# Kernel tuning notes

Measured on AMD Instinct MI355X. Metric: run time of the kernel, lower is better.

## Reference

```python
import math
import jax, jax.numpy as jnp
import numpy as np

D_MODEL, STATE_DIM, SEQ_L = 256, 64, 8192


def setup_inputs() -> dict:
    key = jax.random.key(0)
    ks = jax.random.split(key, 6)
    d, N = D_MODEL, STATE_DIM
    s = 1.0 / math.sqrt(N)
    return {
        "Lambda_re": jax.random.normal(ks[0], (d, N), jnp.float32),
        "Lambda_im": jax.random.normal(ks[1], (d, N), jnp.float32),
        "P_re": jax.random.normal(ks[2], (d, N), jnp.float32) * s,
        "P_im": jax.random.normal(ks[3], (d, N), jnp.float32) * s,
        "B_re": jax.random.normal(ks[4], (d, N), jnp.float32) * s,
        "B_im": jnp.zeros((d, N), jnp.float32),
        "log_dt": jax.random.uniform(ks[5], (d,), jnp.float32,
                                     math.log(1e-3), math.log(0.1)),
        "D": jnp.zeros((d,), jnpp := jnp.float32) if False else jnp.zeros((d,), jnp.float32),
        "L": SEQ_L,
    }


def reference(Lambda_re, Lambda_im, P_re, P_im, B_re, B_im, log_dt, D, L):
    # NPLR / Cauchy-Woodbury S4 kernel (learn_cd=False -> C = B, D is a zero buffer)
    Lam = (-jax.nn.softplus(Lambda_re) + 1j * Lambda_im).astype(jnp.complex64)  # [d, N]
    P = (P_re + 1j * P_im).astype(jnp.complex64)                                # [d, N]
    B = (B_re + 1j * B_im).astype(jnp.complex64)                                # [d, N]
    dt = jnp.exp(log_dt)                                                        # [d]

    k = jnp.arange(L)
    z = jnp.exp((-2j * jnp.pi / L) * k).astype(jnp.complex64)                   # [L] roots of unity
    eps = jnp.finfo(jnp.float32).eps
    denom_z = 1.0 + z
    denom_z = jnp.where(jnp.abs(denom_z) < eps, jnp.complex64(eps), denom_z)

    # Bilinear-transform frequencies g: [d, L] complex
    g = (2.0 / dt)[:, None] * ((1.0 - z) / denom_z)[None, :]

    # Cauchy resolvent R: [d, L, N] complex (the dominant intermediate)
    R = 1.0 / (g[:, :, None] - Lam[:, None, :])

    Pc, Bc = jnp.conj(P), jnp.conj(B)
    PRB = jnp.einsum('dn,dln,dn->dl', Pc, R, B)
    PRP = jnp.einsum('dn,dln,dn->dl', Pc, R, P)
    BRB = jnp.einsum('dn,dln,dn->dl', Bc, R, B)
    BRP = jnp.einsum('dn,dln,dn->dl', Bc, R, P)

    # Woodbury rank-1 correction, then undo the bilinear prefactor
    K_hat = (2.0 / denom_z)[None, :] * (BRB - BRP * PRB / (1.0 + PRP))          # [d, L]
    K = jnp.fft.ifft(K_hat, n=L, axis=-1).real.astype(jnp.float32)
    return (K, D)
```

## Files before the change

kernel.cpp:

```cpp
#include <hip/hip_runtime.h>
#include <math.h>

#ifndef M_PI
#define M_PI 3.14159265358979323846
#endif

#define DMODEL 256
#define NSTATE 64
#define LSEQ   8192
#define INVL   (1.0f/8192.0f)

#define OFF_TW  0
#define OFF_DN  (6144*8)
#define OFF_CDT (OFF_DN + DMODEL*NSTATE*32)

__device__ __forceinline__ float sin_rev(float r) {
#if __has_builtin(__builtin_amdgcn_sinf)
  return __builtin_amdgcn_sinf(r);
#else
  return __sinf(r * 6.283185307179586f);
#endif
}
__device__ __forceinline__ float cos_rev(float r) {
#if __has_builtin(__builtin_amdgcn_cosf)
  return __builtin_amdgcn_cosf(r);
#else
  return __cosf(r * 6.283185307179586f);
#endif
}

__device__ __forceinline__ float2 cmul(float2 a, float2 b) {
  return make_float2(a.x*b.x - a.y*b.y, a.x*b.y + a.y*b.x);
}

__device__ __forceinline__ float2 woodbury(float2 S1, float2 S2, float2 S3,
                                           float2 S4, float T) {
  float nr = (S1.x*S1.x - S1.y*S1.y) + (S2.x*S2.x - S2.y*S2.y);
  float ni = 2.0f*(S1.x*S1.y + S2.x*S2.y);
  float dr = 1.0f + S3.x, di = S3.y;
  float inv = __builtin_amdgcn_rcpf(fmaf(dr, dr, di*di));
  float qr = (nr*dr + ni*di) * inv;
  float qi = (ni*dr - nr*di) * inv;
  float vr = S4.x - qr, vi = S4.y - qi;
  return make_float2((vr - T*vi)*INVL, (vi + T*vr)*INVL);
}

__global__ __launch_bounds__(256) void precompute_kernel(
    const float* __restrict__ Lre, const float* __restrict__ Lim,
    const float* __restrict__ Pre, const float* __restrict__ Pim,
    const float* __restrict__ Bre, const float* __restrict__ Bim,
    const float* __restrict__ log_dt, char* __restrict__ ws)
{
  const int t = blockIdx.x * blockDim.x + threadIdx.x;
  float2* tw  = (float2*)(ws + OFF_TW);
  float4* dn  = (float4*)(ws + OFF_DN);
  float*  cdt = (float*)(ws + OFF_CDT);

  if (t < 6144) {
    double th = (2.0 * M_PI / (double)LSEQ) * (double)t;
    double s, c; sincos(th, &s, &c);
    tw[t] = make_float2((float)c, (float)s);
  }
  {
    float lre = Lre[t], lim = Lim[t];
    float pre = Pre[t], pim = Pim[t];
    float bre = Bre[t], bim = Bim[t];
    float sp = fmaxf(lre, 0.0f) + log1pf(expf(-fabsf(lre)));
    float w1r = pre*bre + pim*bim;
    float w1i = pre*bim - pim*bre;
    float w2  = pre*pre + pim*pim;
    float w3  = bre*bre + bim*bim;
    dn[2*t]   = make_float4(lim, sp, sp*sp, w1r);
    dn[2*t+1] = make_float4(w1i, w2, w3, 0.0f);
  }
  if (t < DMODEL) cdt[t] = 2.0f * expf(-log_dt[t]);
}

__global__ __launch_bounds__(1024) void fused_kernel(
    const float4* __restrict__ dn_all, const float* __restrict__ cdt,
    const float2* __restrict__ tw, const float* __restrict__ Din,
    float* __restrict__ out)
{
  __shared__ __align__(16) float2 xy[LSEQ];
  const int d = blockIdx.x;
  const int t = threadIdx.x;
  const float4* dn = dn_all + (size_t)d * (2*NSTATE);
  const float c = cdt[d];

  for (int it = 0; it < 4; ++it) {
    const int b = t + (it << 10);
    const unsigned p = (unsigned)(2*b);
    const unsigned r = __brev(p) >> 19;
    const int kA = (int)((r & 0x1000u) | ((r & 0x0555u) << 1) | ((r & 0x0AAAu) >> 1));
    const float rev = (float)kA * (1.0f/16384.0f);
    const float sA = sin_rev(rev), cAc = cos_rev(rev);
    float TA = sA * __builtin_amdgcn_rcpf(cAc);
    float TB = -cAc * __builtin_amdgcn_rcpf(sA);
    TA = fminf(fmaxf(TA, -1e7f), 1e7f);
    TB = fminf(fmaxf(TB, -1e7f), 1e7f);
    const float gA = c * TA, gB = c * TB;

    float2 S1a = {0,0}, S2a = {0,0}, S3a = {0,0}, S4a = {0,0};
    float2 S1b = {0,0}, S2b = {0,0}, S3b = {0,0}, S4b = {0,0};
#pragma unroll 8
    for (int n = 0; n < NSTATE; ++n) {
      const float4 a = dn[2*n];
      const float4 w = dn[2*n+1];
      {
        const float dim = gA - a.x;
        const float inv = __builtin_amdgcn_rcpf(fmaf(dim, dim, a.z));
        const float rr = a.y * inv;
        const float di = dim * inv;
        S1a.x = fmaf(a.w, rr, S1a.x);  S1a.y = fmaf(a.w, -di, S1a.y);
        S2a.x = fmaf(w.x, rr, S2a.x);  S2a.y = fmaf(w.x, -di, S2a.y);
        S3a.x = fmaf(w.y, rr, S3a.x);  S3a.y = fmaf(w.y, -di, S3a.y);
        S4a.x = fmaf(w.z, rr, S4a.x);  S4a.y = fmaf(w.z, -di, S4a.y);
      }
      {
        const float dim = gB - a.x;
        const float inv = __builtin_amdgcn_rcpf(fmaf(dim, dim, a.z));
        const float rr = a.y * inv;
        const float di = dim * inv;
        S1b.x = fmaf(a.w, rr, S1b.x);  S1b.y = fmaf(a.w, -di, S1b.y);
        S2b.x = fmaf(w.x, rr, S2b.x);  S2b.y = fmaf(w.x, -di, S2b.y);
        S3b.x = fmaf(w.y, rr, S3b.x);  S3b.y = fmaf(w.y, -di, S3b.y);
        S4b.x = fmaf(w.z, rr, S4b.x);  S4b.y = fmaf(w.z, -di, S4b.y);
      }
    }
    const float2 KA = woodbury(S1a, S2a, S3a, S4a, TA);
    const float2 KB = woodbury(S1b, S2b, S3b, S4b, TB);
    ((float4*)xy)[b] = make_float4(KA.x + KB.x, KA.y + KB.y,
                                   KA.x - KB.x, KA.y - KB.y);
  }
  __syncthreads();

#pragma unroll
  for (int s = 0; s < 6; ++s) {
    const int h = 2 << (2*s);
    const int twsh = 10 - 2*s;
#pragma unroll
    for (int j = 0; j < 2; ++j) {
      const int bb = t + (j << 10);
      const int pos = bb & (h - 1);
      const int i0 = ((bb >> (1 + 2*s)) << (3 + 2*s)) + pos;
      const int ti = pos << twsh;
      const float2 w1 = tw[ti];
      const float2 w2 = tw[2*ti];
      const float2 w3 = tw[3*ti];
      const float2 x0 = xy[i0];
      const float2 x1 = xy[i0 + h];
      const float2 x2 = xy[i0 + 2*h];
      const float2 x3 = xy[i0 + 3*h];
      const float2 t1 = cmul(w1, x1);
      const float2 t2 = cmul(w2, x2);
      const float2 t3 = cmul(w3, x3);
      const float2 u0 = make_float2(x0.x + t2.x, x0.y + t2.y);
      const float2 u1 = make_float2(x0.x - t2.x, x0.y - t2.y);
      const float2 u2 = make_float2(t1.x + t3.x, t1.y + t3.y);
      const float2 vv = make_float2(t1.x - t3.x, t1.y - t3.y);
      xy[i0]         = make_float2(u0.x + u2.x, u0.y + u2.y);
      xy[i0 + h]     = make_float2(u1.x - vv.y, u1.y + vv.x);
      xy[i0 + 2*h]   = make_float2(u0.x - u2.x, u0.y - u2.y);
      xy[i0 + 3*h]   = make_float2(u1.x + vv.y, u1.y - vv.x);
    }
    __syncthreads();
  }

  float* orow = out + (size_t)d * LSEQ;
  for (int i = t; i < LSEQ; i += 1024) orow[i] = xy[i].x;

  if (d == 0 && t < DMODEL) out[(size_t)DMODEL * LSEQ + t] = Din[t];
}

extern "C" void kernel_launch(void* const* d_in, const int* in_sizes, int n_in,
                              void* d_out, int out_size, void* d_ws, size_t ws_size,
                              hipStream_t stream)
{
  const float* Lre    = (const float*)d_in[0];
  const float* Lim    = (const float*)d_in[1];
  const float* Pre    = (const float*)d_in[2];
  const float* Pim    = (const float*)d_in[3];
  const float* Bre    = (const float*)d_in[4];
  const float* Bim    = (const float*)d_in[5];
  const float* log_dt = (const float*)d_in[6];
  const float* Din    = (const float*)d_in[7];
  float* out = (float*)d_out;
  char* ws = (char*)d_ws;

  hipLaunchKernelGGL(precompute_kernel, dim3(64), dim3(256), 0, stream,
                     Lre, Lim, Pre, Pim, Bre, Bim, log_dt, ws);
  hipLaunchKernelGGL(fused_kernel, dim3(DMODEL), dim3(1024), 0, stream,
                     (const float4*)(ws + OFF_DN), (const float*)(ws + OFF_CDT),
                     (const float2*)(ws + OFF_TW), Din, out);
}
```

Before: 123.9 us.

## Split fused Cauchy+FFT kernel into separate Cauchy and FFT kernels

The Cauchy/Woodbury evaluation moves into its own kernel with 2048 blocks of 256 threads, so it no longer depends on the 1024-thread blocks that hold 64KB of shared memory for the FFT. Its spectrum goes to a 16MB workspace buffer. A second kernel reloads that buffer into LDS and runs the radix-4 inverse FFT. The aim is better occupancy and load balance for the compute-heavy Cauchy phase, at the cost of an extra global round trip, one more launch, and a fallback path when the workspace is too small.

```diff
diff --git a/kernel.cpp b/kernel.cpp
--- a/kernel.cpp
+++ b/kernel.cpp
@@ -13,6 +13,8 @@
 #define OFF_TW  0
 #define OFF_DN  (6144*8)
 #define OFF_CDT (OFF_DN + DMODEL*NSTATE*32)
+#define OFF_KH  (OFF_CDT + 1024)
+#define WS_NEED ((size_t)OFF_KH + (size_t)DMODEL*4096*16)
 
 __device__ __forceinline__ float sin_rev(float r) {
 #if __has_builtin(__builtin_amdgcn_sinf)
@@ -74,6 +76,118 @@
     dn[2*t+1] = make_float4(w1i, w2, w3, 0.0f);
   }
   if (t < DMODEL) cdt[t] = 2.0f * expf(-log_dt[t]);
+}
+
+__global__ __launch_bounds__(256) void cauchy_kernel(
+    const float4* __restrict__ dn_all, const float* __restrict__ cdt,
+    float4* __restrict__ kh)
+{
+  const int d   = blockIdx.x >> 3;
+  const int oct = blockIdx.x & 7;
+  const float4* dn = dn_all + (size_t)d * (2*NSTATE);
+  const float c = cdt[d];
+  float4* khd = kh + (size_t)d * 4096;
+
+#pragma unroll
+  for (int it = 0; it < 2; ++it) {
+    const int b = (oct << 9) | (it << 8) | (int)threadIdx.x;
+    const unsigned p = (unsigned)(2*b);
+    const unsigned r = __brev(p) >> 19;
+    const int kA = (int)((r & 0x1000u) | ((r & 0x0555u) << 1) | ((r & 0x0AAAu) >> 1));
+    const float rev = (float)kA * (1.0f/16384.0f);
+    const float sA = sin_rev(rev), cAc = cos_rev(rev);
+    float TA = sA * __builtin_amdgcn_rcpf(cAc);
+    float TB = -cAc * __builtin_amdgcn_rcpf(sA);
+    TA = fminf(fmaxf(TA, -1e7f), 1e7f);
+    TB = fminf(fmaxf(TB, -1e7f), 1e7f);
+    const float gA = c * TA, gB = c * TB;
+
+    float2 S1a = {0,0}, S2a = {0,0}, S3a = {0,0}, S4a = {0,0};
+    float2 S1b = {0,0}, S2b = {0,0}, S3b = {0,0}, S4b = {0,0};
+#pragma unroll 8
+    for (int n = 0; n < NSTATE; ++n) {
+      const float4 a = dn[2*n];
+      const float4 w = dn[2*n+1];
+      {
+        const float dim = gA - a.x;
+        const float inv = __builtin_amdgcn_rcpf(fmaf(dim, dim, a.z));
+        const float rr = a.y * inv;
+        const float di = dim * inv;
+        S1a.x = fmaf(a.w, rr, S1a.x);  S1a.y = fmaf(a.w, -di, S1a.y);
+        S2a.x = fmaf(w.x, rr, S2a.x);  S2a.y = fmaf(w.x, -di, S2a.y);
+        S3a.x = fmaf(w.y, rr, S3a.x);  S3a.y = fmaf(w.y, -di, S3a.y);
+        S4a.x = fmaf(w.z, rr, S4a.x);  S4a.y = fmaf(w.z, -di, S4a.y);
+      }
+      {
+        const float dim = gB - a.x;
+        const float inv = __builtin_amdgcn_rcpf(fmaf(dim, dim, a.z));
+        const float rr = a.y * inv;
+        const float di = dim * inv;
+        S1b.x = fmaf(a.w, rr, S1b.x);  S1b.y = fmaf(a.w, -di, S1b.y);
+        S2b.x = fmaf(w.x, rr, S2b.x);  S2b.y = fmaf(w.x, -di, S2b.y);
+        S3b.x = fmaf(w.y, rr, S3b.x);  S3b.y = fmaf(w.y, -di, S3b.y);
+        S4b.x = fmaf(w.z, rr, S4b.x);  S4b.y = fmaf(w.z, -di, S4b.y);
+      }
+    }
+    const float2 KA = woodbury(S1a, S2a, S3a, S4a, TA);
+    const float2 KB = woodbury(S1b, S2b, S3b, S4b, TB);
+    khd[b] = make_float4(KA.x + KB.x, KA.y + KB.y, KA.x - KB.x, KA.y - KB.y);
+  }
+}
+
+__global__ __launch_bounds__(1024) void fft_kernel(
+    const float4* __restrict__ kh, const float2* __restrict__ tw,
+    const float* __restrict__ Din, float* __restrict__ out)
+{
+  __shared__ __align__(16) float2 xy[LSEQ];
+  const int d = blockIdx.x;
+  const int t = threadIdx.x;
+  const float4* src = kh + (size_t)d * 4096;
+  float4* dst4 = (float4*)xy;
+#pragma unroll
+  for (int j = 0; j < 4; ++j) {
+    const int i = t + (j << 10);
+    dst4[i] = src[i];
+  }
+  __syncthreads();
+
+#pragma unroll
+  for (int s = 0; s < 6; ++s) {
+    const int h = 2 << (2*s);
+    const int twsh = 10 - 2*s;
+#pragma unroll
+    for (int j = 0; j < 2; ++j) {
+      const int bb = t + (j << 10);
+      const int pos = bb & (h - 1);
+      const int i0 = ((bb >> (1 + 2*s)) << (3 + 2*s)) + pos;
+      const int ti = pos << twsh;
+      const float2 w1 = tw[ti];
+      const float2 w2 = tw[2*ti];
+      const float2 w3 = tw[3*ti];
+      const float2 x0 = xy[i0];
+      const float2 x1 = xy[i0 + h];
+      const float2 x2 = xy[i0 + 2*h];
+      const float2 x3 = xy[i0 + 3*h];
+      const float2 t1 = cmul(w1, x1);
+      const float2 t2 = cmul(w2, x2);
+      const float2 t3 = cmul(w3, x3);
+      const float2 u0 = make_float2(x0.x + t2.x, x0.y + t2.y);
+      const float2 u1 = make_float2(x0.x - t2.x, x0.y - t2.y);
+      const float2 u2 = make_float2(t1.x + t3.x, t1.y + t3.y);
+      const float2 vv = make_float2(t1.x - t3.x, t1.y - t3.y);
+      xy[i0]         = make_float2(u0.x + u2.x, u0.y + u2.y);
+      xy[i0 + h]     = make_float2(u1.x - vv.y, u1.y + vv.x);
+      xy[i0 + 2*h]   = make_float2(u0.x - u2.x, u0.y - u2.y);
+      xy[i0 + 3*h]   = make_float2(u1.x + vv.y, u1.y - vv.x);
+    }
+    __syncthreads();
+  }
+
+  float* orow = out + (size_t)d * LSEQ;
+#pragma unroll
+  for (int j = 0; j < 8; ++j) orow[t + (j << 10)] = xy[t + (j << 10)].x;
+
+  if (d == 0 && t < DMODEL) out[(size_t)DMODEL * LSEQ + t] = Din[t];
 }
 
 __global__ __launch_bounds__(1024) void fused_kernel(
@@ -189,7 +303,17 @@
 
   hipLaunchKernelGGL(precompute_kernel, dim3(64), dim3(256), 0, stream,
                      Lre, Lim, Pre, Pim, Bre, Bim, log_dt, ws);
-  hipLaunchKernelGGL(fused_kernel, dim3(DMODEL), dim3(1024), 0, stream,
-                     (const float4*)(ws + OFF_DN), (const float*)(ws + OFF_CDT),
-                     (const float2*)(ws + OFF_TW), Din, out);
-}
+
+  if (ws_size >= WS_NEED) {
+    hipLaunchKernelGGL(cauchy_kernel, dim3(DMODEL * 8), dim3(256), 0, stream,
+                       (const float4*)(ws + OFF_DN), (const float*)(ws + OFF_CDT),
+                       (float4*)(ws + OFF_KH));
+    hipLaunchKernelGGL(fft_kernel, dim3(DMODEL), dim3(1024), 0, stream,
+                       (const float4*)(ws + OFF_KH), (const float2*)(ws + OFF_TW),
+                       Din, out);
+  } else {
+    hipLaunchKernelGGL(fused_kernel, dim3(DMODEL), dim3(1024), 0, stream,
+                       (const float4*)(ws + OFF_DN), (const float*)(ws + OFF_CDT),
+                       (const float2*)(ws + OFF_TW), Din, out);
+  }
+}
```

Result: slower. 132.2 us (+6.7%).

## Interchange Cauchy loops to reuse state coefficients across four frequency pairs

Applied to the files above, without the earlier changes.

The Cauchy sum loop order is swapped so each thread loads the per-state coefficients once and applies them to all four of its frequency pairs, holding 64 float2 accumulators in registers. The precompute step now stores sp-scaled weights, which removes the multiply by the real part (rr = sp*inv) in the inner loop and widens each state record to three float4. The final row copy is fully unrolled. The goal is fewer loads and fewer ALU ops per term, at the cost of much higher register pressure, which with 1024-thread blocks could force spills or lower occupancy.

```diff
diff --git a/kernel.cpp b/kernel.cpp
--- a/kernel.cpp
+++ b/kernel.cpp
@@ -12,7 +12,7 @@
 
 #define OFF_TW  0
 #define OFF_DN  (6144*8)
-#define OFF_CDT (OFF_DN + DMODEL*NSTATE*32)
+#define OFF_CDT (OFF_DN + DMODEL*NSTATE*48)
 
 __device__ __forceinline__ float sin_rev(float r) {
 #if __has_builtin(__builtin_amdgcn_sinf)
@@ -70,8 +70,9 @@
     float w1i = pre*bim - pim*bre;
     float w2  = pre*pre + pim*pim;
     float w3  = bre*bre + bim*bim;
-    dn[2*t]   = make_float4(lim, sp, sp*sp, w1r);
-    dn[2*t+1] = make_float4(w1i, w2, w3, 0.0f);
+    dn[3*t]   = make_float4(lim, sp*sp, w1r, w1i);
+    dn[3*t+1] = make_float4(w2, w3, w1r*sp, w1i*sp);
+    dn[3*t+2] = make_float4(w2*sp, w3*sp, 0.0f, 0.0f);
   }
   if (t < DMODEL) cdt[t] = 2.0f * expf(-log_dt[t]);
 }
@@ -84,53 +85,63 @@
   __shared__ __align__(16) float2 xy[LSEQ];
   const int d = blockIdx.x;
   const int t = threadIdx.x;
-  const float4* dn = dn_all + (size_t)d * (2*NSTATE);
+  const float4* dn = dn_all + (size_t)d * (3*NSTATE);
   const float c = cdt[d];
 
-  for (int it = 0; it < 4; ++it) {
-    const int b = t + (it << 10);
+  float TA[4], TB[4], gA[4], gB[4];
+  float2 S[4][8];
+#pragma unroll
+  for (int j = 0; j < 4; ++j) {
+    const int b = t + (j << 10);
     const unsigned p = (unsigned)(2*b);
     const unsigned r = __brev(p) >> 19;
     const int kA = (int)((r & 0x1000u) | ((r & 0x0555u) << 1) | ((r & 0x0AAAu) >> 1));
     const float rev = (float)kA * (1.0f/16384.0f);
-    const float sA = sin_rev(rev), cAc = cos_rev(rev);
-    float TA = sA * __builtin_amdgcn_rcpf(cAc);
-    float TB = -cAc * __builtin_amdgcn_rcpf(sA);
-    TA = fminf(fmaxf(TA, -1e7f), 1e7f);
-    TB = fminf(fmaxf(TB, -1e7f), 1e7f);
-    const float gA = c * TA, gB = c * TB;
-
-    float2 S1a = {0,0}, S2a = {0,0}, S3a = {0,0}, S4a = {0,0};
-    float2 S1b = {0,0}, S2b = {0,0}, S3b = {0,0}, S4b = {0,0};
-#pragma unroll 8
-    for (int n = 0; n < NSTATE; ++n) {
-      const float4 a = dn[2*n];
-      const float4 w = dn[2*n+1];
+    const float sA = sin_rev(rev), cA = cos_rev(rev);
+    float ta = sA * __builtin_amdgcn_rcpf(cA);
+    float tb = -cA * __builtin_amdgcn_rcpf(sA);
+    ta = fminf(fmaxf(ta, -1e7f), 1e7f);
+    tb = fminf(fmaxf(tb, -1e7f), 1e7f);
+    TA[j] = ta; TB[j] = tb;
+    gA[j] = c * ta; gB[j] = c * tb;
+#pragma unroll
+    for (int q = 0; q < 8; ++q) S[j][q] = make_float2(0.0f, 0.0f);
+  }
+
+#pragma unroll 4
+  for (int n = 0; n < NSTATE; ++n) {
+    const float4 q0 = dn[3*n];
+    const float4 q1 = dn[3*n+1];
+    const float4 q2 = dn[3*n+2];
+#pragma unroll
+    for (int j = 0; j < 4; ++j) {
       {
-        const float dim = gA - a.x;
-        const float inv = __builtin_amdgcn_rcpf(fmaf(dim, dim, a.z));
-        const float rr = a.y * inv;
-        const float di = dim * inv;
-        S1a.x = fmaf(a.w, rr, S1a.x);  S1a.y = fmaf(a.w, -di, S1a.y);
-        S2a.x = fmaf(w.x, rr, S2a.x);  S2a.y = fmaf(w.x, -di, S2a.y);
-        S3a.x = fmaf(w.y, rr, S3a.x);  S3a.y = fmaf(w.y, -di, S3a.y);
-        S4a.x = fmaf(w.z, rr, S4a.x);  S4a.y = fmaf(w.z, -di, S4a.y);
+        const float dim = gA[j] - q0.x;
+        const float inv = __builtin_amdgcn_rcpf(fmaf(dim, dim, q0.y));
+        const float v = dim * inv;
+        S[j][0].x = fmaf(q1.z, inv, S[j][0].x);  S[j][0].y = fmaf(-q0.z, v, S[j][0].y);
+        S[j][1].x = fmaf(q1.w, inv, S[j][1].x);  S[j][1].y = fmaf(-q0.w, v, S[j][1].y);
+        S[j][2].x = fmaf(q2.x, inv, S[j][2].x);  S[j][2].y = fmaf(-q1.x, v, S[j][2].y);
+        S[j][3].x = fmaf(q2.y, inv, S[j][3].x);  S[j][3].y = fmaf(-q1.y, v, S[j][3].y);
       }
       {
-        const float dim = gB - a.x;
-        const float inv = __builtin_amdgcn_rcpf(fmaf(dim, dim, a.z));
-        const float rr = a.y * inv;
-        const float di = dim * inv;
-        S1b.x = fmaf(a.w, rr, S1b.x);  S1b.y = fmaf(a.w, -di, S1b.y);
-        S2b.x = fmaf(w.x, rr, S2b.x);  S2b.y = fmaf(w.x, -di, S2b.y);
-        S3b.x = fmaf(w.y, rr, S3b.x);  S3b.y = fmaf(w.y, -di, S3b.y);
-        S4b.x = fmaf(w.z, rr, S4b.x);  S4b.y = fmaf(w.z, -di, S4b.y);
+        const float dim = gB[j] - q0.x;
+        const float inv = __builtin_amdgcn_rcpf(fmaf(dim, dim, q0.y));
+        const float v = dim * inv;
+        S[j][4].x = fmaf(q1.z, inv, S[j][4].x);  S[j][4].y = fmaf(-q0.z, v, S[j][4].y);
+        S[j][5].x = fmaf(q1.w, inv, S[j][5].x);  S[j][5].y = fmaf(-q0.w, v, S[j][5].y);
+        S[j][6].x = fmaf(q2.x, inv, S[j][6].x);  S[j][6].y = fmaf(-q1.x, v, S[j][6].y);
+        S[j][7].x = fmaf(q2.y, inv, S[j][7].x);  S[j][7].y = fmaf(-q1.y, v, S[j][7].y);
       }
     }
-    const float2 KA = woodbury(S1a, S2a, S3a, S4a, TA);
-    const float2 KB = woodbury(S1b, S2b, S3b, S4b, TB);
-    ((float4*)xy)[b] = make_float4(KA.x + KB.x, KA.y + KB.y,
-                                   KA.x - KB.x, KA.y - KB.y);
+  }
+
+#pragma unroll
+  for (int j = 0; j < 4; ++j) {
+    const float2 KA = woodbury(S[j][0], S[j][1], S[j][2], S[j][3], TA[j]);
+    const float2 KB = woodbury(S[j][4], S[j][5], S[j][6], S[j][7], TB[j]);
+    ((float4*)xy)[t + (j << 10)] = make_float4(KA.x + KB.x, KA.y + KB.y,
+                                               KA.x - KB.x, KA.y - KB.y);
   }
   __syncthreads();
 
@@ -167,7 +178,8 @@
   }
 
   float* orow = out + (size_t)d * LSEQ;
-  for (int i = t; i < LSEQ; i += 1024) orow[i] = xy[i].x;
+#pragma unroll
+  for (int j = 0; j < 8; ++j) orow[t + (j << 10)] = xy[t + (j << 10)].x;
 
   if (d == 0 && t < DMODEL) out[(size_t)DMODEL * LSEQ + t] = Din[t];
 }
```

Measured after the change: 124.9 us. About the same (+0.8%).
